# Optimization experiments

Measured on AMD Instinct MI355X. Metric: run time of the kernel, lower is better.

## Reference

```python
import jax, jax.numpy as jnp
import numpy as np

N_NODES = 100000
N_REL = 6
E_PER_REL = 100000
HID = 256
EMB = 256
N_GRAPHS = 128
N_NODE_TYPES = 4
SUBTYPE_BUCKETS = 256


def setup_inputs() -> dict:
    key = jax.random.key(0)
    ks = jax.random.split(key, 20)
    s = 0.05
    return {
        "x_type": jax.random.randint(ks[0], (N_NODES,), 0, N_NODE_TYPES),
        "x_sub": jax.random.randint(ks[1], (N_NODES,), 0, SUBTYPE_BUCKETS),
        "edges": jax.random.randint(ks[2], (N_REL, 2, E_PER_REL), 0, N_NODES),
        "batch_ids": jnp.sort(jax.random.randint(ks[3], (N_NODES,), 0, N_GRAPHS)),
        "n_graphs": N_GRAPHS,
        "type_emb": jax.random.normal(ks[4], (N_NODE_TYPES, HID // 2), jnp.float32) * s,
        "sub_emb": jax.random.normal(ks[5], (SUBTYPE_BUCKETS, HID // 2), jnp.float32) * s,
        "W_rel0": jax.random.normal(ks[6], (N_REL, HID, HID), jnp.float32) * s,
        "W_self0": jax.random.normal(ks[7], (HID, HID), jnp.float32) * s,
        "b0": jnp.zeros((HID,), jnp.float32),
        "W_rel1": jax.random.normal(ks[8], (N_REL, HID, HID), jnp.float32) * s,
        "W_self1": jax.random.normal(ks[9], (HID, HID), jnp.float32) * s,
        "b1": jnp.zeros((HID,), jnp.float32),
        "pW1": jax.random.normal(ks[10], (HID, HID), jnp.float32) * s,
        "pb1": jnp.zeros((HID,), jnp.float32),
        "pW2": jax.random.normal(ks[11], (HID, EMB), jnp.float32) * s,
        "pb2": jnp.zeros((EMB,), jnp.float32),
    }


def _rgcn_layer(h, edges, W_rel, W_self, b, n):
    # edges: (R, 2, E); h: (N, H)
    src, tgt = edges[:, 0, :], edges[:, 1, :]  # (R, E)
    # per-relation gather -> matmul: (R, E, H) @ (R, H, D) -> (R, E, D)
    msg = jnp.einsum('reh,rhd->red', h[src], W_rel)
    tgt_flat = tgt.reshape(-1)
    out = jax.ops.segment_sum(msg.reshape(-1, msg.shape[-1]), tgt_flat, num_segments=n)
    total_deg = jax.ops.segment_sum(jnp.ones_like(tgt_flat, dtype=h.dtype), tgt_flat, num_segments=n)
    total_deg = jnp.clip(total_deg, 1.0)[:, None]
    out = out / total_deg + h @ W_self + b
    return jax.nn.relu(out)


def _mean_pool(h, batch_ids, n_graphs):
    summed = jax.ops.segment_sum(h, batch_ids, num_segments=n_graphs)
    count = jax.ops.segment_sum(jnp.ones((h.shape[0],), h.dtype), batch_ids, num_segments=n_graphs)
    return summed / jnp.clip(count, 1.0)[:, None]


def reference(x_type, x_sub, edges, batch_ids, n_graphs, type_emb, sub_emb,
              W_rel0, W_self0, b0, W_rel1, W_self1, b1, pW1, pb1, pW2, pb2):
    n = x_type.shape[0]
    h = jnp.concatenate([type_emb[x_type], sub_emb[x_sub]], axis=-1)  # (N, HID)
    h = _rgcn_layer(h, edges, W_rel0, W_self0, b0, n)
    h = _rgcn_layer(h, edges, W_rel1, W_self1, b1, n)
    pooled = _mean_pool(h, batch_ids, n_graphs)  # (G, HID)
    return jax.nn.relu(pooled @ pW1 + pb1) @ pW2 + pb2  # (G, EMB)
```

## Files before the change

kernel.cpp:

```cpp
#include <hip/hip_runtime.h>

#define NN    100000
#define NEDGE 100000
#define NRELS 6
#define HIDD  256
#define NGR   128
#define NKEY  (NRELS * NN)
#define NEDGT (NRELS * NEDGE)
#define WFRAG_ELEMS (4 * 7 * 16 * 2 * 64 * 8)
#define SMASK 0xFFFFF
#define NSHARD 8

typedef __bf16 bf16;
typedef __bf16 bf16x4 __attribute__((ext_vector_type(4)));
typedef __bf16 bf16x8 __attribute__((ext_vector_type(8)));
typedef float  f32x4  __attribute__((ext_vector_type(4)));
typedef float  f32x16 __attribute__((ext_vector_type(16)));

__device__ __forceinline__ float readlane_f(float v, int sl) {
    return __int_as_float(__builtin_amdgcn_readlane(__float_as_int(v), sl));
}

__global__ __launch_bounds__(256)
void hist_kernel(const int* __restrict__ edges, int* __restrict__ hist)
{
    int i = blockIdx.x * 256 + threadIdx.x;
    if (i >= NEDGT) return;
    int r = i / NEDGE;
    int e = i - r * NEDGE;
    int t = edges[r * (2 * NEDGE) + NEDGE + e];
    atomicAdd(&hist[r * NN + t], 1);
}

__global__ __launch_bounds__(256)
void scan_l0(const int* __restrict__ in, int* __restrict__ out, int* __restrict__ bsum, int n)
{
    __shared__ int sdata[256];
    const int t = threadIdx.x;
    const int base = blockIdx.x * 2048 + t * 8;
    int v[8]; int s = 0;
#pragma unroll
    for (int i = 0; i < 8; ++i) {
        int idx = base + i;
        int x = (idx < n) ? in[idx] : 0;
        v[i] = s; s += x;
    }
    sdata[t] = s;
    __syncthreads();
    for (int off = 1; off < 256; off <<= 1) {
        int y = (t >= off) ? sdata[t - off] : 0;
        __syncthreads();
        sdata[t] += y;
        __syncthreads();
    }
    int excl = sdata[t] - s;
#pragma unroll
    for (int i = 0; i < 8; ++i) {
        int idx = base + i;
        if (idx < n) out[idx] = excl + v[i];
    }
    if (t == 0) bsum[blockIdx.x] = sdata[255];
}

__global__ __launch_bounds__(256)
void scan_l1(int* __restrict__ bsum, int n)
{
    __shared__ int sdata[256];
    const int t = threadIdx.x;
    const int base = t * 8;
    int v[8]; int s = 0;
#pragma unroll
    for (int i = 0; i < 8; ++i) {
        int idx = base + i;
        int x = (idx < n) ? bsum[idx] : 0;
        v[i] = s; s += x;
    }
    sdata[t] = s;
    __syncthreads();
    for (int off = 1; off < 256; off <<= 1) {
        int y = (t >= off) ? sdata[t - off] : 0;
        __syncthreads();
        sdata[t] += y;
        __syncthreads();
    }
    int excl = sdata[t] - s;
#pragma unroll
    for (int i = 0; i < 8; ++i) {
        int idx = base + i;
        if (idx < n) bsum[idx] = excl + v[i];
    }
}

__global__ __launch_bounds__(256)
void scan_l2(int* __restrict__ offs, int* __restrict__ cursor, const int* __restrict__ bsum,
             const int* __restrict__ hist, float* __restrict__ invdeg,
             const int* __restrict__ batch_ids, float* __restrict__ cnt, int n)
{
    int idx = blockIdx.x * 256 + threadIdx.x;
    if (idx == 0) offs[NKEY] = NEDGT;

    {
        const int lane = threadIdx.x & 63;
        const bool valid = idx < NN;
        const int gv = valid ? batch_ids[idx] : -1;
        const int gprev = __shfl(gv, lane - 1);
        const bool head = valid && (lane == 0 || gv != gprev);
        const bool stop = head || !valid;
        const unsigned long long mask = __ballot(stop);
        if (head) {
            unsigned long long above = (lane == 63) ? 0ull : (mask >> (lane + 1));
            const int next = above ? (lane + 1 + __builtin_ctzll(above)) : 64;
            atomicAdd(&cnt[gv], (float)(next - lane));
        }
    }

    if (idx < NN) {
        int d = 0;
#pragma unroll
        for (int r = 0; r < NRELS; ++r) d += hist[r * NN + idx];
        invdeg[idx] = 1.0f / fmaxf((float)d, 1.0f);
    }
    if (idx >= n) return;
    int v = offs[idx] + bsum[idx >> 11];
    offs[idx] = v;
    cursor[idx] = v;
}

__global__ __launch_bounds__(256)
void scatter_kernel(const int* __restrict__ edges, int* __restrict__ cursor,
                    const int* __restrict__ xt, const int* __restrict__ xs,
                    int* __restrict__ epack, int* __restrict__ epack2)
{
    int i = blockIdx.x * 256 + threadIdx.x;
    if (i >= NEDGT) return;
    int r = i / NEDGE;
    int e = i - r * NEDGE;
    int s = edges[r * (2 * NEDGE) + e];
    int t = edges[r * (2 * NEDGE) + NEDGE + e];
    int pos = atomicAdd(&cursor[r * NN + t], 1);
    epack[pos] = s | ((t & 15) << 20);
    epack2[pos] = xt[s] * 256 + xs[s];
}

__global__ __launch_bounds__(256)
void build_etab(const float* __restrict__ temb, const float* __restrict__ semb,
                bf16* __restrict__ etab)
{
    const int c = blockIdx.x;
    const int f = threadIdx.x;
    const int t = c >> 8, s = c & 255;
    float v = (f < 128) ? temb[t * 128 + f] : semb[s * 128 + (f - 128)];
    etab[c * 256 + f] = (bf16)v;
}

__global__ __launch_bounds__(256)
void build_wfrag(const float* __restrict__ Wr0, const float* __restrict__ Ws0,
                 const float* __restrict__ Wr1, const float* __restrict__ Ws1,
                 bf16* __restrict__ Wf0, bf16* __restrict__ Wf1)
{
    const int seg = blockIdx.x;
    const int step = blockIdx.y;
    const int layer = blockIdx.z;
    const int tid = threadIdx.x;
    const int w = tid >> 6;
    const int lane = tid & 63;
    const int l31 = lane & 31;
    const int lhi = lane >> 5;

    const float* Wr = layer ? Wr1 : Wr0;
    const float* Ws = layer ? Ws1 : Ws0;
    const float* src = (seg < 6) ? (Wr + ((size_t)seg << 16)) : Ws;
    bf16* Wf = layer ? Wf1 : Wf0;

    const int kb = step * 16 + lhi * 8;
#pragma unroll
    for (int ct = 0; ct < 2; ++ct) {
        const int n = w * 64 + ct * 32 + l31;
        bf16x8 o;
#pragma unroll
        for (int j = 0; j < 8; ++j)
            o[j] = (bf16)src[(size_t)(kb + j) * 256 + n];
        const size_t fb_idx = (size_t)(((w * 7 + seg) * 16 + step) * 2 + ct) * 64 + lane;
        *(bf16x8*)(Wf + fb_idx * 8) = o;
    }
}

template<bool L0, bool POOL>
__global__ __launch_bounds__(256, 3)
void rgcn_fused(const bf16* __restrict__ hin,
                const int* __restrict__ xt, const int* __restrict__ xs,
                const float* __restrict__ temb, const float* __restrict__ semb,
                const bf16* __restrict__ Wfrag, const float* __restrict__ bias,
                const float* __restrict__ invdeg, const int* __restrict__ offs,
                const int* __restrict__ epack, const int* __restrict__ epack2,
                const int* __restrict__ batch_ids,
                float* __restrict__ pooled, bf16* __restrict__ hout)
{
    constexpr int DEPTH = 16;
    const int m0 = blockIdx.x * 64;
    const int tid = threadIdx.x;
    const int lane = tid & 63;
    const int w = tid >> 6;
    const int l31 = lane & 31;
    const int lhi = lane >> 5;
    const int rbase = w * 16;

    __shared__ __align__(16) bf16 As[64 * HIDD];

    f32x16 acc[2][2] = {};

    int ivrow = m0 + rbase + (lane & 15);
    if (ivrow >= NN) ivrow = NN - 1;
    const float ivreg = invdeg[ivrow];

    for (int seg = 0; seg < 7; ++seg) {
        __syncthreads();

#pragma unroll
        for (int z = 0; z < 8; ++z) {
            const int row = rbase + lhi * 8 + z;
            const int unit = row * 32 + (l31 ^ (row & 7));
            *(bf16x8*)&As[unit * 8] = (bf16x8)(bf16)0.0f;
        }

        if (seg == 6) {
#pragma unroll
            for (int z = 0; z < 8; ++z) {
                const int row = rbase + lhi * 8 + z;
                const int gr = m0 + row;
                if (gr < NN) {
                    bf16x8 o;
                    if (L0) {
                        const int f0 = l31 * 8;
                        const float* src = (f0 < 128) ? (temb + xt[gr] * 128 + f0)
                                                      : (semb + xs[gr] * 128 + (f0 - 128));
                        f32x4 x0 = *(const f32x4*)src;
                        f32x4 x1 = *(const f32x4*)(src + 4);
                        o[0] = (bf16)x0[0]; o[1] = (bf16)x0[1];
                        o[2] = (bf16)x0[2]; o[3] = (bf16)x0[3];
                        o[4] = (bf16)x1[0]; o[5] = (bf16)x1[1];
                        o[6] = (bf16)x1[2]; o[7] = (bf16)x1[3];
                    } else {
                        o = *(const bf16x8*)(hin + ((size_t)gr << 8) + l31 * 8);
                    }
                    const int unit = row * 32 + (l31 ^ (row & 7));
                    *(bf16x8*)&As[unit * 8] = o;
                }
            }
        } else {
            const int gr0 = m0 + rbase;
            if (gr0 < NN) {
                const int rend = (gr0 + 16 < NN) ? (gr0 + 16) : NN;
                int st = offs[seg * NN + gr0];
                const int en = offs[seg * NN + rend];

                float a0 = 0.f, a1 = 0.f, a2 = 0.f, a3 = 0.f;
                int cur = -1;

                while (st < en) {
                    const int cnt = (en - st < 64) ? (en - st) : 64;
                    const int idx = st + ((lane < cnt) ? lane : (cnt - 1));
                    const int pv = epack[idx];
                    const int rv = L0 ? epack2[idx]
                                      : (pv & SMASK);

                    for (int base = 0; base < cnt; base += DEPTH) {
                        bf16x4 hb[DEPTH];
#pragma unroll
                        for (int p = 0; p < DEPTH; ++p) {
                            int ip = base + p;
                            ip = (ip < cnt) ? ip : (cnt - 1);
                            const int s = __builtin_amdgcn_readlane(rv, ip);
                            hb[p] = *(const bf16x4*)(hin + ((size_t)s << 8) + lane * 4);
                        }
#pragma unroll
                        for (int p = 0; p < DEPTH; ++p) {
                            if (base + p < cnt) {
                                const int t = __builtin_amdgcn_readlane(pv, base + p) >> 20;
                                if (t != cur) {
                                    if (cur >= 0) {
                                        const float inv = readlane_f(ivreg, cur);
                                        bf16x4 o;
                                        o.x = (bf16)(a0 * inv); o.y = (bf16)(a1 * inv);
                                        o.z = (bf16)(a2 * inv); o.w = (bf16)(a3 * inv);
                                        const int row = rbase + cur;
                                        const int unit = row * 32 + ((lane >> 1) ^ (row & 7));
                                        *(bf16x4*)&As[unit * 8 + (lane & 1) * 4] = o;
                                    }
                                    cur = t; a0 = a1 = a2 = a3 = 0.f;
                                }
                                a0 += (float)hb[p].x; a1 += (float)hb[p].y;
                                a2 += (float)hb[p].z; a3 += (float)hb[p].w;
                            }
                        }
                    }
                    st += cnt;
                }
                if (cur >= 0) {
                    const float inv = readlane_f(ivreg, cur);
                    bf16x4 o;
                    o.x = (bf16)(a0 * inv); o.y = (bf16)(a1 * inv);
                    o.z = (bf16)(a2 * inv); o.w = (bf16)(a3 * inv);
                    const int row = rbase + cur;
                    const int unit = row * 32 + ((lane >> 1) ^ (row & 7));
                    *(bf16x4*)&As[unit * 8 + (lane & 1) * 4] = o;
                }
            }
        }

        __syncthreads();

        const bf16* const wseg = Wfrag + ((size_t)((w * 7 + seg) * 16) * 2 * 64) * 8;
#pragma unroll
        for (int step = 0; step < 16; ++step) {
            bf16x8 b0 = *(const bf16x8*)(wseg + ((size_t)(step * 2 + 0) * 64 + lane) * 8);
            bf16x8 b1 = *(const bf16x8*)(wseg + ((size_t)(step * 2 + 1) * 64 + lane) * 8);
            const int ku = step * 2 + lhi;
            bf16x8 a0 = *(const bf16x8*)&As[(l31 * 32 + (ku ^ (l31 & 7))) * 8];
            bf16x8 a1 = *(const bf16x8*)&As[((32 + l31) * 32 + (ku ^ (l31 & 7))) * 8];
            acc[0][0] = __builtin_amdgcn_mfma_f32_32x32x16_bf16(a0, b0, acc[0][0], 0, 0, 0);
            acc[0][1] = __builtin_amdgcn_mfma_f32_32x32x16_bf16(a0, b1, acc[0][1], 0, 0, 0);
            acc[1][0] = __builtin_amdgcn_mfma_f32_32x32x16_bf16(a1, b0, acc[1][0], 0, 0, 0);
            acc[1][1] = __builtin_amdgcn_mfma_f32_32x32x16_bf16(a1, b1, acc[1][1], 0, 0, 0);
        }
    }

    float bcol[2];
#pragma unroll
    for (int ct = 0; ct < 2; ++ct) bcol[ct] = bias[w * 64 + ct * 32 + l31];

    if constexpr (POOL) {
        float* pshard = pooled + (size_t)(blockIdx.x & (NSHARD - 1)) * NGR * HIDD;
        __syncthreads();
        int* bidArr = (int*)As;
        if (tid < 64) {
            const int r = m0 + tid;
            bidArr[tid] = (r < NN) ? batch_ids[r] : -1;
        }
        __syncthreads();
        const int last = (m0 + 63 < NN) ? 63 : (NN - 1 - m0);
        const int glo = bidArr[0];
        const int ghi = bidArr[last];
        for (int g = glo; g <= ghi; ++g) {
            float s0 = 0.f, s1 = 0.f;
#pragma unroll
            for (int rt = 0; rt < 2; ++rt) {
#pragma unroll
                for (int reg = 0; reg < 16; ++reg) {
                    const int rl = rt * 32 + (reg & 3) + 8 * (reg >> 2) + 4 * lhi;
                    if (bidArr[rl] == g) {
                        s0 += fmaxf(acc[rt][0][reg] + bcol[0], 0.0f);
                        s1 += fmaxf(acc[rt][1][reg] + bcol[1], 0.0f);
                    }
                }
            }
            s0 += __shfl_xor(s0, 32);
            s1 += __shfl_xor(s1, 32);
            if (lhi == 0) {
                atomicAdd(&pshard[g * HIDD + w * 64 + l31], s0);
                atomicAdd(&pshard[g * HIDD + w * 64 + 32 + l31], s1);
            }
        }
    } else {
#pragma unroll
        for (int rt = 0; rt < 2; ++rt) {
#pragma unroll
            for (int reg = 0; reg < 16; ++reg) {
                const int row = m0 + rt * 32 + (reg & 3) + 8 * (reg >> 2) + 4 * lhi;
                if (row < NN) {
#pragma unroll
                    for (int ct = 0; ct < 2; ++ct) {
                        const int col = w * 64 + ct * 32 + l31;
                        float v = acc[rt][ct][reg] + bcol[ct];
                        hout[((size_t)row << 8) + col] = (bf16)fmaxf(v, 0.0f);
                    }
                }
            }
        }
    }
}

__global__ __launch_bounds__(256)
void mlp_kernel(const float* __restrict__ pooled, const float* __restrict__ cnt,
                const float* __restrict__ pW1, const float* __restrict__ pb1,
                const float* __restrict__ pW2, const float* __restrict__ pb2,
                float* __restrict__ out)
{
    const int g = blockIdx.x;
    const int d = threadIdx.x;
    __shared__ float pn[HIDD];
    __shared__ float mid[HIDD];
    float c = fmaxf(cnt[g], 1.0f);
    float sacc = 0.f;
#pragma unroll
    for (int x = 0; x < NSHARD; ++x)
        sacc += pooled[(size_t)x * NGR * HIDD + g * HIDD + d];
    pn[d] = sacc / c;
    __syncthreads();
    float s = pb1[d];
    for (int k = 0; k < HIDD; ++k) s = fmaf(pn[k], pW1[k * HIDD + d], s);
    mid[d] = fmaxf(s, 0.0f);
    __syncthreads();
    float s2 = pb2[d];
    for (int k = 0; k < HIDD; ++k) s2 = fmaf(mid[k], pW2[k * HIDD + d], s2);
    out[g * HIDD + d] = s2;
}

extern "C" void kernel_launch(void* const* d_in, const int* in_sizes, int n_in,
                              void* d_out, int out_size, void* d_ws, size_t ws_size,
                              hipStream_t stream)
{
    const int*   x_type    = (const int*)d_in[0];
    const int*   x_sub     = (const int*)d_in[1];
    const int*   edges     = (const int*)d_in[2];
    const int*   batch_ids = (const int*)d_in[3];
    const float* type_emb  = (const float*)d_in[5];
    const float* sub_emb   = (const float*)d_in[6];
    const float* W_rel0    = (const float*)d_in[7];
    const float* W_self0   = (const float*)d_in[8];
    const float* b0        = (const float*)d_in[9];
    const float* W_rel1    = (const float*)d_in[10];
    const float* W_self1   = (const float*)d_in[11];
    const float* b1        = (const float*)d_in[12];
    const float* pW1       = (const float*)d_in[13];
    const float* pb1       = (const float*)d_in[14];
    const float* pW2       = (const float*)d_in[15];
    const float* pb2       = (const float*)d_in[16];
    float* out = (float*)d_out;

    char* p = (char*)d_ws;
    auto carve = [&](size_t bytes) { char* q = p; p += (bytes + 255) & ~255ull; return q; };
    bf16*  h1     = (bf16*) carve((size_t)NN * HIDD * sizeof(bf16));
    bf16*  Wf0    = (bf16*) carve((size_t)WFRAG_ELEMS * sizeof(bf16));
    bf16*  Wf1    = (bf16*) carve((size_t)WFRAG_ELEMS * sizeof(bf16));
    bf16*  etab   = (bf16*) carve((size_t)1024 * 256 * sizeof(bf16));
    float* invdeg = (float*)carve((size_t)NN * sizeof(float));
    int*   hist   = (int*)  carve((size_t)NKEY * sizeof(int));
    int*   offs   = (int*)  carve((size_t)(NKEY + 1) * sizeof(int));
    int*   cursor = (int*)  carve((size_t)NKEY * sizeof(int));
    int*   bsum   = (int*)  carve(2048 * sizeof(int));
    int*   epack  = (int*)  carve((size_t)NEDGT * sizeof(int));
    int*   epack2 = (int*)  carve((size_t)NEDGT * sizeof(int));
    float* pooled = (float*)carve((size_t)NSHARD * NGR * HIDD * sizeof(float));
    float* cnt    = (float*)carve((size_t)NGR * sizeof(float));

    hipMemsetAsync(hist, 0, (size_t)NKEY * sizeof(int), stream);
    hipMemsetAsync(pooled, 0, (size_t)(NSHARD * NGR * HIDD + NGR) * sizeof(float), stream);

    const int NB0 = (NKEY + 2047) / 2048;
    hist_kernel<<<(NEDGT + 255) / 256, 256, 0, stream>>>(edges, hist);
    scan_l0<<<NB0, 256, 0, stream>>>(hist, offs, bsum, NKEY);
    scan_l1<<<1, 256, 0, stream>>>(bsum, NB0);
    scan_l2<<<(NKEY + 255) / 256, 256, 0, stream>>>(offs, cursor, bsum, hist, invdeg,
                                                    batch_ids, cnt, NKEY);
    scatter_kernel<<<(NEDGT + 255) / 256, 256, 0, stream>>>(edges, cursor, x_type, x_sub,
                                                            epack, epack2);
    build_etab<<<1024, 256, 0, stream>>>(type_emb, sub_emb, etab);

    dim3 wgrid(7, 16, 2);
    build_wfrag<<<wgrid, 256, 0, stream>>>(W_rel0, W_self0, W_rel1, W_self1, Wf0, Wf1);

    const int FGRID = (NN + 63) / 64;
    rgcn_fused<true, false><<<FGRID, 256, 0, stream>>>(
        etab, x_type, x_sub, type_emb, sub_emb,
        Wf0, b0, invdeg, offs, epack, epack2, batch_ids, pooled, h1);
    rgcn_fused<false, true><<<FGRID, 256, 0, stream>>>(
        h1, x_type, x_sub, type_emb, sub_emb,
        Wf1, b1, invdeg, offs, epack, epack2, batch_ids, pooled, nullptr);

    mlp_kernel<<<NGR, 256, 0, stream>>>(pooled, cnt, pW1, pb1, pW2, pb2, out);
}
```

Measured before the change: 543.5 us.

## Use 8 waves per block in fused RGCN, halving rows and columns per wave

The fused RGCN kernel now launches 512 threads (8 waves) per 64-row tile instead of 256. Each wave gathers and aggregates edges for 8 rows instead of 16, and computes one 32-column MFMA slice instead of two, so each wave carries half the accumulators. The edge pack now stores the target row mod 64 so any wave can place its rows in shared memory. The aim is more waves in flight to hide gather latency. The trade-off is that each wave re-reads the A tile from shared memory for fewer columns, and register pressure is tighter under launch_bounds(512,4).

```diff
diff --git a/kernel.cpp b/kernel.cpp
--- a/kernel.cpp
+++ b/kernel.cpp
@@ -138,7 +138,7 @@
     int s = edges[r * (2 * NEDGE) + e];
     int t = edges[r * (2 * NEDGE) + NEDGE + e];
     int pos = atomicAdd(&cursor[r * NN + t], 1);
-    epack[pos] = s | ((t & 15) << 20);
+    epack[pos] = s | ((t & 63) << 20);
     epack2[pos] = xt[s] * 256 + xs[s];
 }
 
@@ -186,7 +186,7 @@
 }
 
 template<bool L0, bool POOL>
-__global__ __launch_bounds__(256, 3)
+__global__ __launch_bounds__(512, 4)
 void rgcn_fused(const bf16* __restrict__ hin,
                 const int* __restrict__ xt, const int* __restrict__ xs,
                 const float* __restrict__ temb, const float* __restrict__ semb,
@@ -203,13 +203,14 @@
     const int w = tid >> 6;
     const int l31 = lane & 31;
     const int lhi = lane >> 5;
-    const int rbase = w * 16;
+    const int rbase = w * 8;
+    const int wc = (w >> 1) * 64 + (w & 1) * 32;
 
     __shared__ __align__(16) bf16 As[64 * HIDD];
 
-    f32x16 acc[2][2] = {};
-
-    int ivrow = m0 + rbase + (lane & 15);
+    f32x16 acc[2] = {};
+
+    int ivrow = m0 + rbase + (lane & 7);
     if (ivrow >= NN) ivrow = NN - 1;
     const float ivreg = invdeg[ivrow];
 
@@ -217,16 +218,16 @@
         __syncthreads();
 
 #pragma unroll
-        for (int z = 0; z < 8; ++z) {
-            const int row = rbase + lhi * 8 + z;
+        for (int z = 0; z < 4; ++z) {
+            const int row = rbase + z * 2 + lhi;
             const int unit = row * 32 + (l31 ^ (row & 7));
             *(bf16x8*)&As[unit * 8] = (bf16x8)(bf16)0.0f;
         }
 
         if (seg == 6) {
 #pragma unroll
-            for (int z = 0; z < 8; ++z) {
-                const int row = rbase + lhi * 8 + z;
+            for (int z = 0; z < 4; ++z) {
+                const int row = rbase + z * 2 + lhi;
                 const int gr = m0 + row;
                 if (gr < NN) {
                     bf16x8 o;
@@ -250,7 +251,7 @@
         } else {
             const int gr0 = m0 + rbase;
             if (gr0 < NN) {
-                const int rend = (gr0 + 16 < NN) ? (gr0 + 16) : NN;
+                const int rend = (gr0 + 8 < NN) ? (gr0 + 8) : NN;
                 int st = offs[seg * NN + gr0];
                 const int en = offs[seg * NN + rend];
 
@@ -276,15 +277,14 @@
 #pragma unroll
                         for (int p = 0; p < DEPTH; ++p) {
                             if (base + p < cnt) {
-                                const int t = __builtin_amdgcn_readlane(pv, base + p) >> 20;
+                                const int t = (__builtin_amdgcn_readlane(pv, base + p) >> 20) & 63;
                                 if (t != cur) {
                                     if (cur >= 0) {
-                                        const float inv = readlane_f(ivreg, cur);
+                                        const float inv = readlane_f(ivreg, cur - rbase);
                                         bf16x4 o;
                                         o.x = (bf16)(a0 * inv); o.y = (bf16)(a1 * inv);
                                         o.z = (bf16)(a2 * inv); o.w = (bf16)(a3 * inv);
-                                        const int row = rbase + cur;
-                                        const int unit = row * 32 + ((lane >> 1) ^ (row & 7));
+                                        const int unit = cur * 32 + ((lane >> 1) ^ (cur & 7));
                                         *(bf16x4*)&As[unit * 8 + (lane & 1) * 4] = o;
                                     }
                                     cur = t; a0 = a1 = a2 = a3 = 0.f;
@@ -297,12 +297,11 @@
                     st += cnt;
                 }
                 if (cur >= 0) {
-                    const float inv = readlane_f(ivreg, cur);
+                    const float inv = readlane_f(ivreg, cur - rbase);
                     bf16x4 o;
                     o.x = (bf16)(a0 * inv); o.y = (bf16)(a1 * inv);
                     o.z = (bf16)(a2 * inv); o.w = (bf16)(a3 * inv);
-                    const int row = rbase + cur;
-                    const int unit = row * 32 + ((lane >> 1) ^ (row & 7));
+                    const int unit = cur * 32 + ((lane >> 1) ^ (cur & 7));
                     *(bf16x4*)&As[unit * 8 + (lane & 1) * 4] = o;
                 }
             }
@@ -310,24 +309,19 @@
 
         __syncthreads();
 
-        const bf16* const wseg = Wfrag + ((size_t)((w * 7 + seg) * 16) * 2 * 64) * 8;
+        const bf16* const wseg = Wfrag + ((size_t)(((w >> 1) * 7 + seg) * 16) * 2 * 64) * 8;
 #pragma unroll
         for (int step = 0; step < 16; ++step) {
-            bf16x8 b0 = *(const bf16x8*)(wseg + ((size_t)(step * 2 + 0) * 64 + lane) * 8);
-            bf16x8 b1 = *(const bf16x8*)(wseg + ((size_t)(step * 2 + 1) * 64 + lane) * 8);
+            bf16x8 b0 = *(const bf16x8*)(wseg + ((size_t)(step * 2 + (w & 1)) * 64 + lane) * 8);
             const int ku = step * 2 + lhi;
             bf16x8 a0 = *(const bf16x8*)&As[(l31 * 32 + (ku ^ (l31 & 7))) * 8];
             bf16x8 a1 = *(const bf16x8*)&As[((32 + l31) * 32 + (ku ^ (l31 & 7))) * 8];
-            acc[0][0] = __builtin_amdgcn_mfma_f32_32x32x16_bf16(a0, b0, acc[0][0], 0, 0, 0);
-            acc[0][1] = __builtin_amdgcn_mfma_f32_32x32x16_bf16(a0, b1, acc[0][1], 0, 0, 0);
-            acc[1][0] = __builtin_amdgcn_mfma_f32_32x32x16_bf16(a1, b0, acc[1][0], 0, 0, 0);
-            acc[1][1] = __builtin_amdgcn_mfma_f32_32x32x16_bf16(a1, b1, acc[1][1], 0, 0, 0);
-        }
-    }
-
-    float bcol[2];
-#pragma unroll
-    for (int ct = 0; ct < 2; ++ct) bcol[ct] = bias[w * 64 + ct * 32 + l31];
+            acc[0] = __builtin_amdgcn_mfma_f32_32x32x16_bf16(a0, b0, acc[0], 0, 0, 0);
+            acc[1] = __builtin_amdgcn_mfma_f32_32x32x16_bf16(a1, b0, acc[1], 0, 0, 0);
+        }
+    }
+
+    const float bcol = bias[wc + l31];
 
     if constexpr (POOL) {
         float* pshard = pooled + (size_t)(blockIdx.x & (NSHARD - 1)) * NGR * HIDD;
@@ -342,24 +336,19 @@
         const int glo = bidArr[0];
         const int ghi = bidArr[last];
         for (int g = glo; g <= ghi; ++g) {
-            float s0 = 0.f, s1 = 0.f;
+            float s0 = 0.f;
 #pragma unroll
             for (int rt = 0; rt < 2; ++rt) {
 #pragma unroll
                 for (int reg = 0; reg < 16; ++reg) {
                     const int rl = rt * 32 + (reg & 3) + 8 * (reg >> 2) + 4 * lhi;
-                    if (bidArr[rl] == g) {
-                        s0 += fmaxf(acc[rt][0][reg] + bcol[0], 0.0f);
-                        s1 += fmaxf(acc[rt][1][reg] + bcol[1], 0.0f);
-                    }
+                    if (bidArr[rl] == g)
+                        s0 += fmaxf(acc[rt][reg] + bcol, 0.0f);
                 }
             }
             s0 += __shfl_xor(s0, 32);
-            s1 += __shfl_xor(s1, 32);
-            if (lhi == 0) {
-                atomicAdd(&pshard[g * HIDD + w * 64 + l31], s0);
-                atomicAdd(&pshard[g * HIDD + w * 64 + 32 + l31], s1);
-            }
+            if (lhi == 0)
+                atomicAdd(&pshard[g * HIDD + wc + l31], s0);
         }
     } else {
 #pragma unroll
@@ -368,12 +357,9 @@
             for (int reg = 0; reg < 16; ++reg) {
                 const int row = m0 + rt * 32 + (reg & 3) + 8 * (reg >> 2) + 4 * lhi;
                 if (row < NN) {
-#pragma unroll
-                    for (int ct = 0; ct < 2; ++ct) {
-                        const int col = w * 64 + ct * 32 + l31;
-                        float v = acc[rt][ct][reg] + bcol[ct];
-                        hout[((size_t)row << 8) + col] = (bf16)fmaxf(v, 0.0f);
-                    }
+                    const int col = wc + l31;
+                    float v = acc[rt][reg] + bcol;
+                    hout[((size_t)row << 8) + col] = (bf16)fmaxf(v, 0.0f);
                 }
             }
         }
@@ -461,10 +447,10 @@
     build_wfrag<<<wgrid, 256, 0, stream>>>(W_rel0, W_self0, W_rel1, W_self1, Wf0, Wf1);
 
     const int FGRID = (NN + 63) / 64;
-    rgcn_fused<true, false><<<FGRID, 256, 0, stream>>>(
+    rgcn_fused<true, false><<<FGRID, 512, 0, stream>>>(
         etab, x_type, x_sub, type_emb, sub_emb,
         Wf0, b0, invdeg, offs, epack, epack2, batch_ids, pooled, h1);
-    rgcn_fused<false, true><<<FGRID, 256, 0, stream>>>(
+    rgcn_fused<false, true><<<FGRID, 512, 0, stream>>>(
         h1, x_type, x_sub, type_emb, sub_emb,
         Wf1, b1, invdeg, offs, epack, epack2, batch_ids, pooled, nullptr);
 
```

After: 533.4 us. No clear change (-1.9%).
